# Kernel optimization log

Hardware: AMD Instinct MI355X
Metric: run time of the kernel (lower is better)

Reference implementation:

```python
import jax, jax.numpy as jnp
import numpy as np

BS, NS, S = 4, 16384, 8
C_PLANE, RES = 64, 128
IN_DIM = 3 * C_PLANE  # 192


def _bilerp(plane, uv):
    """plane: [B,C,H,W]; uv: [B,n,2] in [0,1] -> [B,n,C] bilinear samples (border clamp)."""
    B, C, H, W = plane.shape
    x = jnp.clip(uv[..., 0], 0.0, 1.0) * (W - 1)
    y = jnp.clip(uv[..., 1], 0.0, 1.0) * (H - 1)
    x0 = jnp.floor(x).astype(jnp.int32)
    y0 = jnp.floor(y).astype(jnp.int32)
    x1 = jnp.minimum(x0 + 1, W - 1)
    y1 = jnp.minimum(y0 + 1, H - 1)
    wx = (x - x0)[:, :, None]
    wy = (y - y0)[:, :, None]
    gat = jax.vmap(lambda p, yy, xx: p[:, yy, xx].T)  # per-batch gather -> [n,C]
    f00 = gat(plane, y0, x0)
    f01 = gat(plane, y0, x1)
    f10 = gat(plane, y1, x0)
    f11 = gat(plane, y1, x1)
    return (f00 * (1 - wx) * (1 - wy) + f01 * wx * (1 - wy)
            + f10 * (1 - wx) * wy + f11 * wx * wy)


def _sample_triplane(p, feat_xz, feat_xy, feat_yz):
    """p: [B,n,3] -> concat of bilinear samples from the three planes: [B,n,3C]."""
    f_xz = _bilerp(feat_xz, p[..., jnp.array([0, 2])])
    f_xy = _bilerp(feat_xy, p[..., jnp.array([0, 1])])
    f_yz = _bilerp(feat_yz, p[..., jnp.array([1, 2])])
    return jnp.concatenate([f_xz, f_xy, f_yz], axis=-1)


def setup_inputs() -> dict:
    key = jax.random.key(0)
    ks = jax.random.split(key, 12)
    w = 0.05  # small init so predicted offsets stay near the query point
    return {
        "query_pos": jax.random.uniform(ks[0], (BS, NS, 3), dtype=jnp.float32),
        "feat_xz": jax.random.normal(ks[1], (BS, C_PLANE, RES, RES), dtype=jnp.float32),
        "feat_xy": jax.random.normal(ks[2], (BS, C_PLANE, RES, RES), dtype=jnp.float32),
        "feat_yz": jax.random.normal(ks[3], (BS, C_PLANE, RES, RES), dtype=jnp.float32),
        "W_v": jax.random.normal(ks[4], (IN_DIM, IN_DIM), dtype=jnp.float32) * w,
        "b_v": jnp.zeros((IN_DIM,), jnp.float32),
        "W_out": jax.random.normal(ks[5], (IN_DIM, IN_DIM), dtype=jnp.float32) * w,
        "b_out": jnp.zeros((IN_DIM,), jnp.float32),
        "W_off": jax.random.normal(ks[6], (3 * S, IN_DIM), dtype=jnp.float32) * w,
        "b_off": jnp.zeros((3 * S,), jnp.float32),
        "W_wt": jax.random.normal(ks[7], (S, IN_DIM), dtype=jnp.float32) * w,
        "b_wt": jnp.zeros((S,), jnp.float32),
    }


def reference(query_pos, feat_xz, feat_xy, feat_yz, W_v, b_v, W_out, b_out,
              W_off, b_off, W_wt, b_wt):
    bs, ns, _ = query_pos.shape
    # feature at query points: [bs, ns, IN_DIM]
    feature = _sample_triplane(query_pos, feat_xz, feat_xy, feat_yz)
    # predicted per-sample offsets and weights
    off = (feature @ W_off.T + b_off).reshape(bs, ns, S, 3)
    wt = (feature @ W_wt.T + b_wt)[..., None]            # [bs, ns, S, 1]
    pts = off + query_pos[:, :, None, :]                  # [bs, ns, S, 3]
    # gather features at offset locations: [bs, ns*S, IN_DIM]
    aux = _sample_triplane(pts.reshape(bs, ns * S, 3), feat_xz, feat_xy, feat_yz)
    v = (aux @ W_v.T + b_v).reshape(bs, ns, S, -1)        # [bs, ns, S, hidden]
    out = (v * wt).sum(axis=-2)                           # weighted sum over samples
    out = out @ W_out.T + b_out + feature                 # residual add
    return out  # [bs, ns, IN_DIM]
```

## Files before the change

### kernel.cpp

```cpp
#include <hip/hip_runtime.h>

#define BS 4
#define NS 16384
#define S_SAMP 8
#define CPL 64
#define RES 128
#define IN_DIM 192
#define NPTS (BS * NS)
#define PL_STRIDE (RES * RES * CPL)
#define PLANES_T_FLOATS (BS * 3 * PL_STRIDE)

__global__ __launch_bounds__(256) void transpose_planes(
    const float* __restrict__ xz, const float* __restrict__ xy,
    const float* __restrict__ yz, float* __restrict__ T) {
  __shared__ float tile[64][33];
  int blk = blockIdx.x;
  int xt = blk & 3;
  int y  = (blk >> 2) & 127;
  int pl = (blk >> 9) % 3;
  int b  = blk / 1536;
  const float* src = (pl == 0) ? xz : ((pl == 1) ? xy : yz);
  src += (size_t)b * CPL * RES * RES + (size_t)y * RES + xt * 32;
  int tid = threadIdx.x;
  int xl = tid & 31, c0 = tid >> 5;
#pragma unroll
  for (int r = 0; r < 8; ++r) {
    int c = c0 + (r << 3);
    tile[c][xl] = src[(size_t)c * RES * RES + xl];
  }
  __syncthreads();
  float* dst = T + ((size_t)(b * 3 + pl) * RES * RES + (size_t)y * RES + xt * 32) * CPL;
  int c2 = tid & 63, x0 = tid >> 6;
#pragma unroll
  for (int r = 0; r < 8; ++r) {
    int xl2 = x0 + (r << 2);
    dst[(size_t)xl2 * CPL + c2] = tile[c2][xl2];
  }
}

__global__ __launch_bounds__(192) void precompute_wc(
    const float* __restrict__ W_v, const float* __restrict__ b_v,
    const float* __restrict__ W_out, float* __restrict__ WcT,
    float* __restrict__ bc) {
  int j = threadIdx.x;
  int k = blockIdx.x;
  if (k < IN_DIM) {
    float acc = 0.f;
    for (int m = 0; m < IN_DIM; ++m)
      acc += W_out[j * IN_DIM + m] * W_v[m * IN_DIM + k];
    WcT[k * IN_DIM + j] = acc;
  } else {
    float acc = 0.f;
    for (int m = 0; m < IN_DIM; ++m)
      acc += W_out[j * IN_DIM + m] * b_v[m];
    bc[j] = acc;
  }
}

__device__ __forceinline__ float bilerp_s(const float* __restrict__ pb, float u,
                                          float v, int lane) {
  u = fminf(fmaxf(u, 0.f), 1.f) * 127.f;
  v = fminf(fmaxf(v, 0.f), 1.f) * 127.f;
  float xf = floorf(u), yf = floorf(v);
  float wx = u - xf, wy = v - yf;
  int x0 = __builtin_amdgcn_readfirstlane((int)xf);
  int y0 = __builtin_amdgcn_readfirstlane((int)yf);
  int dx = (x0 < 127) ? CPL : 0;
  int dy = (y0 < 127) ? RES * CPL : 0;
  const float* b00 = pb + (((y0 << 7) + x0) << 6);
  float f00 = b00[lane];
  float f01 = b00[dx + lane];
  float f10 = b00[dy + lane];
  float f11 = b00[dy + dx + lane];
  float fx0 = f00 + wx * (f01 - f00);
  float fx1 = f10 + wx * (f11 - f10);
  return fx0 + wy * (fx1 - fx0);
}

__global__ __launch_bounds__(256, 4) void fused_sample(
    const float* __restrict__ qpos, const float* __restrict__ planesT,
    const float* __restrict__ W_off, const float* __restrict__ b_off,
    const float* __restrict__ W_wt, const float* __restrict__ b_wt,
    float* __restrict__ waux, float* __restrict__ swtg,
    float* __restrict__ featg) {
  __shared__ float feat_lds[4][IN_DIM];
  __shared__ float offwt[4][32];
  int w = threadIdx.x >> 6, lane = threadIdx.x & 63;
  int p = (blockIdx.x << 2) + w;
  int b = p >> 14;
  float qx = qpos[p * 3 + 0], qy = qpos[p * 3 + 1], qz = qpos[p * 3 + 2];
  const float* Tb = planesT + (size_t)b * 3 * PL_STRIDE;

  float f0 = bilerp_s(Tb, qx, qz, lane);
  float f1 = bilerp_s(Tb + PL_STRIDE, qx, qy, lane);
  float f2 = bilerp_s(Tb + 2 * PL_STRIDE, qy, qz, lane);
  feat_lds[w][lane] = f0;
  feat_lds[w][64 + lane] = f1;
  feat_lds[w][128 + lane] = f2;
  __syncthreads();

  {
    int oj = lane & 31;
    const float* row = (oj < 24) ? (W_off + oj * IN_DIM)
                                 : (W_wt + (oj - 24) * IN_DIM);
    float bias = (oj < 24) ? b_off[oj] : b_wt[oj - 24];
    int k0 = (lane >> 5) * 96;
    const float4* r4 = (const float4*)(row + k0);
    float a0 = 0.f, a1 = 0.f, a2 = 0.f, a3 = 0.f;
#pragma unroll
    for (int k4 = 0; k4 < 24; ++k4) {
      float4 rv = r4[k4];
      a0 += rv.x * feat_lds[w][k0 + 4 * k4 + 0];
      a1 += rv.y * feat_lds[w][k0 + 4 * k4 + 1];
      a2 += rv.z * feat_lds[w][k0 + 4 * k4 + 2];
      a3 += rv.w * feat_lds[w][k0 + 4 * k4 + 3];
    }
    float acc = (a0 + a1) + (a2 + a3);
    acc += __shfl_xor(acc, 32);
    if (lane < 32) offwt[w][oj] = acc + bias;
  }
  __syncthreads();

  float wa0 = 0.f, wa1 = 0.f, wa2 = 0.f, swt = 0.f;
#pragma unroll 4
  for (int s = 0; s < S_SAMP; ++s) {
    float wt = offwt[w][24 + s];
    float px = qx + offwt[w][3 * s + 0];
    float py = qy + offwt[w][3 * s + 1];
    float pz = qz + offwt[w][3 * s + 2];
    wa0 += wt * bilerp_s(Tb, px, pz, lane);
    wa1 += wt * bilerp_s(Tb + PL_STRIDE, px, py, lane);
    wa2 += wt * bilerp_s(Tb + 2 * PL_STRIDE, py, pz, lane);
    swt += wt;
  }

  size_t o = (size_t)p * IN_DIM + lane;
  waux[o] = wa0; waux[o + 64] = wa1; waux[o + 128] = wa2;
  if (lane == 0) swtg[p] = swt;
  featg[o] = f0; featg[o + 64] = f1; featg[o + 128] = f2;
}

__global__ __launch_bounds__(512) void out_gemm(
    const float* __restrict__ waux, const float* __restrict__ swtg,
    const float* __restrict__ WcT, const float* __restrict__ bc,
    const float* __restrict__ b_out, float* __restrict__ out) {
  __shared__ float wtile[64 * IN_DIM];
  int tid = threadIdx.x;
  int w = tid >> 6, lane = tid & 63;
  int p0 = blockIdx.x * 128 + w * 16;

  float acc[4][4][3] = {};
  for (int c = 0; c < 3; ++c) {
#pragma unroll
    for (int r = 0; r < 24; ++r)
      wtile[tid + r * 512] = WcT[c * 64 * IN_DIM + tid + r * 512];
    __syncthreads();
#pragma unroll
    for (int g = 0; g < 4; ++g) {
      const float* wrow[4];
#pragma unroll
      for (int q = 0; q < 4; ++q)
        wrow[q] = waux +
                  (size_t)__builtin_amdgcn_readfirstlane(p0 + g * 4 + q) * IN_DIM +
                  c * 64;
#pragma unroll 4
      for (int k = 0; k < 64; ++k) {
        float v0 = wtile[k * IN_DIM + lane];
        float v1 = wtile[k * IN_DIM + 64 + lane];
        float v2 = wtile[k * IN_DIM + 128 + lane];
#pragma unroll
        for (int q = 0; q < 4; ++q) {
          float wv = wrow[q][k];
          acc[g][q][0] += v0 * wv;
          acc[g][q][1] += v1 * wv;
          acc[g][q][2] += v2 * wv;
        }
      }
    }
    __syncthreads();
  }
#pragma unroll
  for (int g = 0; g < 4; ++g)
#pragma unroll
    for (int q = 0; q < 4; ++q) {
      int p = p0 + g * 4 + q;
      float sw = swtg[p];
#pragma unroll
      for (int t = 0; t < 3; ++t) {
        int j = lane + t * 64;
        size_t o = (size_t)p * IN_DIM + j;
        out[o] = acc[g][q][t] + sw * bc[j] + b_out[j] + out[o];
      }
    }
}

extern "C" void kernel_launch(void* const* d_in, const int* in_sizes, int n_in,
                              void* d_out, int out_size, void* d_ws,
                              size_t ws_size, hipStream_t stream) {
  const float* qpos  = (const float*)d_in[0];
  const float* xz    = (const float*)d_in[1];
  const float* xy    = (const float*)d_in[2];
  const float* yz    = (const float*)d_in[3];
  const float* W_v   = (const float*)d_in[4];
  const float* b_v   = (const float*)d_in[5];
  const float* W_out = (const float*)d_in[6];
  const float* b_out = (const float*)d_in[7];
  const float* W_off = (const float*)d_in[8];
  const float* b_off = (const float*)d_in[9];
  const float* W_wt  = (const float*)d_in[10];
  const float* b_wt  = (const float*)d_in[11];

  float* ws      = (float*)d_ws;
  float* planesT = ws;
  float* waux    = planesT + PLANES_T_FLOATS;
  float* swtg    = waux + (size_t)NPTS * IN_DIM;
  float* WcT     = swtg + NPTS;
  float* bc      = WcT + IN_DIM * IN_DIM;
  float* out     = (float*)d_out;

  hipLaunchKernelGGL(transpose_planes, dim3(BS * 3 * RES * 4), dim3(256), 0,
                     stream, xz, xy, yz, planesT);
  hipLaunchKernelGGL(precompute_wc, dim3(IN_DIM + 1), dim3(IN_DIM), 0, stream,
                     W_v, b_v, W_out, WcT, bc);
  hipLaunchKernelGGL(fused_sample, dim3(NPTS / 4), dim3(256), 0, stream, qpos,
                     planesT, W_off, b_off, W_wt, b_wt, waux, swtg, out);
  hipLaunchKernelGGL(out_gemm, dim3(NPTS / 128), dim3(512), 0, stream, waux,
                     swtg, WcT, bc, b_out, out);
}
```

Measured before the change: 484.6 us.

## Process two points per wave in sampler and restage output GEMM tiles

The sampling kernel now handles two query points per wavefront and issues all 24 bilinear corner loads before interpolating, to expose more memory-level parallelism. The offset/weight projection gives each half-wave a full 192-length dot product, which removes the cross-lane shuffle. The output GEMM now stages a 64-point activation tile in LDS and streams WcT rows from global memory, replacing the earlier staging of weight tiles. precompute_wc swaps its block and thread indices so that W_v reads coalesce. The extra in-flight loads raise register pressure and may lower occupancy.

```diff
diff --git a/kernel.cpp b/kernel.cpp
--- a/kernel.cpp
+++ b/kernel.cpp
@@ -42,9 +42,9 @@
     const float* __restrict__ W_v, const float* __restrict__ b_v,
     const float* __restrict__ W_out, float* __restrict__ WcT,
     float* __restrict__ bc) {
-  int j = threadIdx.x;
-  int k = blockIdx.x;
-  if (k < IN_DIM) {
+  int j = blockIdx.x;
+  int k = threadIdx.x;
+  if (j < IN_DIM) {
     float acc = 0.f;
     for (int m = 0; m < IN_DIM; ++m)
       acc += W_out[j * IN_DIM + m] * W_v[m * IN_DIM + k];
@@ -52,29 +52,24 @@
   } else {
     float acc = 0.f;
     for (int m = 0; m < IN_DIM; ++m)
-      acc += W_out[j * IN_DIM + m] * b_v[m];
-    bc[j] = acc;
-  }
-}
-
-__device__ __forceinline__ float bilerp_s(const float* __restrict__ pb, float u,
-                                          float v, int lane) {
+      acc += W_out[k * IN_DIM + m] * b_v[m];
+    bc[k] = acc;
+  }
+}
+
+__device__ __forceinline__ void mkaddr(const float* __restrict__ pb, float u,
+                                       float v, const float*& b00, int& dx,
+                                       int& dy, float& wx, float& wy) {
   u = fminf(fmaxf(u, 0.f), 1.f) * 127.f;
   v = fminf(fmaxf(v, 0.f), 1.f) * 127.f;
   float xf = floorf(u), yf = floorf(v);
-  float wx = u - xf, wy = v - yf;
+  wx = u - xf;
+  wy = v - yf;
   int x0 = __builtin_amdgcn_readfirstlane((int)xf);
   int y0 = __builtin_amdgcn_readfirstlane((int)yf);
-  int dx = (x0 < 127) ? CPL : 0;
-  int dy = (y0 < 127) ? RES * CPL : 0;
-  const float* b00 = pb + (((y0 << 7) + x0) << 6);
-  float f00 = b00[lane];
-  float f01 = b00[dx + lane];
-  float f10 = b00[dy + lane];
-  float f11 = b00[dy + dx + lane];
-  float fx0 = f00 + wx * (f01 - f00);
-  float fx1 = f10 + wx * (f11 - f10);
-  return fx0 + wy * (fx1 - fx0);
+  dx = (x0 < 127) ? CPL : 0;
+  dy = (y0 < 127) ? RES * CPL : 0;
+  b00 = pb + (((y0 << 7) + x0) << 6);
 }
 
 __global__ __launch_bounds__(256, 4) void fused_sample(
@@ -83,115 +78,176 @@
     const float* __restrict__ W_wt, const float* __restrict__ b_wt,
     float* __restrict__ waux, float* __restrict__ swtg,
     float* __restrict__ featg) {
-  __shared__ float feat_lds[4][IN_DIM];
-  __shared__ float offwt[4][32];
+  __shared__ float feat_lds[8][IN_DIM];
+  __shared__ float offwt[8][32];
   int w = threadIdx.x >> 6, lane = threadIdx.x & 63;
-  int p = (blockIdx.x << 2) + w;
-  int b = p >> 14;
-  float qx = qpos[p * 3 + 0], qy = qpos[p * 3 + 1], qz = qpos[p * 3 + 2];
-  const float* Tb = planesT + (size_t)b * 3 * PL_STRIDE;
-
-  float f0 = bilerp_s(Tb, qx, qz, lane);
-  float f1 = bilerp_s(Tb + PL_STRIDE, qx, qy, lane);
-  float f2 = bilerp_s(Tb + 2 * PL_STRIDE, qy, qz, lane);
-  feat_lds[w][lane] = f0;
-  feat_lds[w][64 + lane] = f1;
-  feat_lds[w][128 + lane] = f2;
-  __syncthreads();
-
+  int p0 = blockIdx.x * 8 + w * 2;
+  int p1 = p0 + 1;
+  int b0 = p0 >> 14, b1 = p1 >> 14;
+  float qx0 = qpos[p0 * 3 + 0], qy0 = qpos[p0 * 3 + 1], qz0 = qpos[p0 * 3 + 2];
+  float qx1 = qpos[p1 * 3 + 0], qy1 = qpos[p1 * 3 + 1], qz1 = qpos[p1 * 3 + 2];
+  const float* Tb0 = planesT + (size_t)b0 * 3 * PL_STRIDE;
+  const float* Tb1 = planesT + (size_t)b1 * 3 * PL_STRIDE;
+
+  float f[6];
   {
-    int oj = lane & 31;
+    const float* B[6]; int DX[6], DY[6]; float WX[6], WY[6];
+    mkaddr(Tb0,                 qx0, qz0, B[0], DX[0], DY[0], WX[0], WY[0]);
+    mkaddr(Tb0 + PL_STRIDE,     qx0, qy0, B[1], DX[1], DY[1], WX[1], WY[1]);
+    mkaddr(Tb0 + 2 * PL_STRIDE, qy0, qz0, B[2], DX[2], DY[2], WX[2], WY[2]);
+    mkaddr(Tb1,                 qx1, qz1, B[3], DX[3], DY[3], WX[3], WY[3]);
+    mkaddr(Tb1 + PL_STRIDE,     qx1, qy1, B[4], DX[4], DY[4], WX[4], WY[4]);
+    mkaddr(Tb1 + 2 * PL_STRIDE, qy1, qz1, B[5], DX[5], DY[5], WX[5], WY[5]);
+    float t00[6], t01[6], t10[6], t11[6];
+#pragma unroll
+    for (int i = 0; i < 6; ++i) {
+      t00[i] = B[i][lane];
+      t01[i] = B[i][DX[i] + lane];
+      t10[i] = B[i][DY[i] + lane];
+      t11[i] = B[i][DY[i] + DX[i] + lane];
+    }
+#pragma unroll
+    for (int i = 0; i < 6; ++i) {
+      float a = t00[i] + WX[i] * (t01[i] - t00[i]);
+      float c = t10[i] + WX[i] * (t11[i] - t10[i]);
+      f[i] = a + WY[i] * (c - a);
+    }
+  }
+  feat_lds[w * 2 + 0][lane] = f[0];
+  feat_lds[w * 2 + 0][64 + lane] = f[1];
+  feat_lds[w * 2 + 0][128 + lane] = f[2];
+  feat_lds[w * 2 + 1][lane] = f[3];
+  feat_lds[w * 2 + 1][64 + lane] = f[4];
+  feat_lds[w * 2 + 1][128 + lane] = f[5];
+  __syncthreads();
+
+  {
+    int pt = lane >> 5, oj = lane & 31;
     const float* row = (oj < 24) ? (W_off + oj * IN_DIM)
                                  : (W_wt + (oj - 24) * IN_DIM);
     float bias = (oj < 24) ? b_off[oj] : b_wt[oj - 24];
-    int k0 = (lane >> 5) * 96;
-    const float4* r4 = (const float4*)(row + k0);
+    const float4* r4 = (const float4*)row;
+    const float4* fl = (const float4*)feat_lds[w * 2 + pt];
     float a0 = 0.f, a1 = 0.f, a2 = 0.f, a3 = 0.f;
 #pragma unroll
-    for (int k4 = 0; k4 < 24; ++k4) {
+    for (int k4 = 0; k4 < IN_DIM / 4; ++k4) {
       float4 rv = r4[k4];
-      a0 += rv.x * feat_lds[w][k0 + 4 * k4 + 0];
-      a1 += rv.y * feat_lds[w][k0 + 4 * k4 + 1];
-      a2 += rv.z * feat_lds[w][k0 + 4 * k4 + 2];
-      a3 += rv.w * feat_lds[w][k0 + 4 * k4 + 3];
-    }
-    float acc = (a0 + a1) + (a2 + a3);
-    acc += __shfl_xor(acc, 32);
-    if (lane < 32) offwt[w][oj] = acc + bias;
-  }
-  __syncthreads();
-
-  float wa0 = 0.f, wa1 = 0.f, wa2 = 0.f, swt = 0.f;
-#pragma unroll 4
+      float4 fv = fl[k4];
+      a0 += rv.x * fv.x;
+      a1 += rv.y * fv.y;
+      a2 += rv.z * fv.z;
+      a3 += rv.w * fv.w;
+    }
+    offwt[w * 2 + pt][oj] = bias + ((a0 + a1) + (a2 + a3));
+  }
+  __syncthreads();
+
+  float wa[2][3] = {};
+  float swt0 = 0.f, swt1 = 0.f;
+#pragma unroll 2
   for (int s = 0; s < S_SAMP; ++s) {
-    float wt = offwt[w][24 + s];
-    float px = qx + offwt[w][3 * s + 0];
-    float py = qy + offwt[w][3 * s + 1];
-    float pz = qz + offwt[w][3 * s + 2];
-    wa0 += wt * bilerp_s(Tb, px, pz, lane);
-    wa1 += wt * bilerp_s(Tb + PL_STRIDE, px, py, lane);
-    wa2 += wt * bilerp_s(Tb + 2 * PL_STRIDE, py, pz, lane);
-    swt += wt;
-  }
-
-  size_t o = (size_t)p * IN_DIM + lane;
-  waux[o] = wa0; waux[o + 64] = wa1; waux[o + 128] = wa2;
-  if (lane == 0) swtg[p] = swt;
-  featg[o] = f0; featg[o + 64] = f1; featg[o + 128] = f2;
-}
-
-__global__ __launch_bounds__(512) void out_gemm(
+    float ox0 = offwt[w * 2 + 0][3 * s + 0];
+    float oy0 = offwt[w * 2 + 0][3 * s + 1];
+    float oz0 = offwt[w * 2 + 0][3 * s + 2];
+    float wt0 = offwt[w * 2 + 0][24 + s];
+    float ox1 = offwt[w * 2 + 1][3 * s + 0];
+    float oy1 = offwt[w * 2 + 1][3 * s + 1];
+    float oz1 = offwt[w * 2 + 1][3 * s + 2];
+    float wt1 = offwt[w * 2 + 1][24 + s];
+    float px0 = qx0 + ox0, py0 = qy0 + oy0, pz0 = qz0 + oz0;
+    float px1 = qx1 + ox1, py1 = qy1 + oy1, pz1 = qz1 + oz1;
+
+    const float* B[6]; int DX[6], DY[6]; float WX[6], WY[6];
+    mkaddr(Tb0,                 px0, pz0, B[0], DX[0], DY[0], WX[0], WY[0]);
+    mkaddr(Tb0 + PL_STRIDE,     px0, py0, B[1], DX[1], DY[1], WX[1], WY[1]);
+    mkaddr(Tb0 + 2 * PL_STRIDE, py0, pz0, B[2], DX[2], DY[2], WX[2], WY[2]);
+    mkaddr(Tb1,                 px1, pz1, B[3], DX[3], DY[3], WX[3], WY[3]);
+    mkaddr(Tb1 + PL_STRIDE,     px1, py1, B[4], DX[4], DY[4], WX[4], WY[4]);
+    mkaddr(Tb1 + 2 * PL_STRIDE, py1, pz1, B[5], DX[5], DY[5], WX[5], WY[5]);
+    float t00[6], t01[6], t10[6], t11[6];
+#pragma unroll
+    for (int i = 0; i < 6; ++i) {
+      t00[i] = B[i][lane];
+      t01[i] = B[i][DX[i] + lane];
+      t10[i] = B[i][DY[i] + lane];
+      t11[i] = B[i][DY[i] + DX[i] + lane];
+    }
+    float r[6];
+#pragma unroll
+    for (int i = 0; i < 6; ++i) {
+      float a = t00[i] + WX[i] * (t01[i] - t00[i]);
+      float c = t10[i] + WX[i] * (t11[i] - t10[i]);
+      r[i] = a + WY[i] * (c - a);
+    }
+    wa[0][0] += wt0 * r[0]; wa[0][1] += wt0 * r[1]; wa[0][2] += wt0 * r[2];
+    wa[1][0] += wt1 * r[3]; wa[1][1] += wt1 * r[4]; wa[1][2] += wt1 * r[5];
+    swt0 += wt0; swt1 += wt1;
+  }
+
+  size_t o0 = (size_t)p0 * IN_DIM + lane;
+  size_t o1 = (size_t)p1 * IN_DIM + lane;
+  waux[o0] = wa[0][0]; waux[o0 + 64] = wa[0][1]; waux[o0 + 128] = wa[0][2];
+  waux[o1] = wa[1][0]; waux[o1 + 64] = wa[1][1]; waux[o1 + 128] = wa[1][2];
+  if (lane == 0) { swtg[p0] = swt0; swtg[p1] = swt1; }
+  featg[o0] = f[0]; featg[o0 + 64] = f[1]; featg[o0 + 128] = f[2];
+  featg[o1] = f[3]; featg[o1 + 64] = f[4]; featg[o1 + 128] = f[5];
+}
+
+__global__ __launch_bounds__(256) void out_gemm(
     const float* __restrict__ waux, const float* __restrict__ swtg,
     const float* __restrict__ WcT, const float* __restrict__ bc,
     const float* __restrict__ b_out, float* __restrict__ out) {
-  __shared__ float wtile[64 * IN_DIM];
+  __shared__ float at[64 * IN_DIM];
   int tid = threadIdx.x;
   int w = tid >> 6, lane = tid & 63;
-  int p0 = blockIdx.x * 128 + w * 16;
-
-  float acc[4][4][3] = {};
+  int p0 = blockIdx.x * 64;
+
+  const float4* src = (const float4*)(waux + (size_t)p0 * IN_DIM);
+  float4* dst4 = (float4*)at;
+#pragma unroll
+  for (int i = 0; i < 12; ++i) dst4[tid + i * 256] = src[tid + i * 256];
+  __syncthreads();
+
+  int pw = w * 16;
+  float acc[16][3] = {};
   for (int c = 0; c < 3; ++c) {
-#pragma unroll
-    for (int r = 0; r < 24; ++r)
-      wtile[tid + r * 512] = WcT[c * 64 * IN_DIM + tid + r * 512];
-    __syncthreads();
-#pragma unroll
-    for (int g = 0; g < 4; ++g) {
-      const float* wrow[4];
-#pragma unroll
-      for (int q = 0; q < 4; ++q)
-        wrow[q] = waux +
-                  (size_t)__builtin_amdgcn_readfirstlane(p0 + g * 4 + q) * IN_DIM +
-                  c * 64;
-#pragma unroll 4
-      for (int k = 0; k < 64; ++k) {
-        float v0 = wtile[k * IN_DIM + lane];
-        float v1 = wtile[k * IN_DIM + 64 + lane];
-        float v2 = wtile[k * IN_DIM + 128 + lane];
-#pragma unroll
-        for (int q = 0; q < 4; ++q) {
-          float wv = wrow[q][k];
-          acc[g][q][0] += v0 * wv;
-          acc[g][q][1] += v1 * wv;
-          acc[g][q][2] += v2 * wv;
-        }
+    const float* wc = WcT + c * 64 * IN_DIM;
+#pragma unroll 2
+    for (int k4 = 0; k4 < 16; ++k4) {
+      float v0[4], v1[4], v2[4];
+#pragma unroll
+      for (int kk = 0; kk < 4; ++kk) {
+        const float* r = wc + (k4 * 4 + kk) * IN_DIM;
+        v0[kk] = r[lane];
+        v1[kk] = r[64 + lane];
+        v2[kk] = r[128 + lane];
       }
-    }
-    __syncthreads();
-  }
-#pragma unroll
-  for (int g = 0; g < 4; ++g)
-#pragma unroll
-    for (int q = 0; q < 4; ++q) {
-      int p = p0 + g * 4 + q;
-      float sw = swtg[p];
-#pragma unroll
-      for (int t = 0; t < 3; ++t) {
-        int j = lane + t * 64;
-        size_t o = (size_t)p * IN_DIM + j;
-        out[o] = acc[g][q][t] + sw * bc[j] + b_out[j] + out[o];
+#pragma unroll
+      for (int q = 0; q < 16; ++q) {
+        float4 a4 = *(const float4*)&at[(pw + q) * IN_DIM + c * 64 + k4 * 4];
+        acc[q][0] += v0[0] * a4.x + v0[1] * a4.y + v0[2] * a4.z + v0[3] * a4.w;
+        acc[q][1] += v1[0] * a4.x + v1[1] * a4.y + v1[2] * a4.z + v1[3] * a4.w;
+        acc[q][2] += v2[0] * a4.x + v2[1] * a4.y + v2[2] * a4.z + v2[3] * a4.w;
       }
     }
+  }
+
+  float bcv[3], bov[3];
+#pragma unroll
+  for (int t = 0; t < 3; ++t) {
+    bcv[t] = bc[lane + t * 64];
+    bov[t] = b_out[lane + t * 64];
+  }
+#pragma unroll
+  for (int q = 0; q < 16; ++q) {
+    int p = p0 + pw + q;
+    float sw = swtg[p];
+#pragma unroll
+    for (int t = 0; t < 3; ++t) {
+      size_t o = (size_t)p * IN_DIM + lane + t * 64;
+      out[o] = acc[q][t] + sw * bcv[t] + bov[t] + out[o];
+    }
+  }
 }
 
 extern "C" void kernel_launch(void* const* d_in, const int* in_sizes, int n_in,
@@ -222,8 +278,8 @@
                      stream, xz, xy, yz, planesT);
   hipLaunchKernelGGL(precompute_wc, dim3(IN_DIM + 1), dim3(IN_DIM), 0, stream,
                      W_v, b_v, W_out, WcT, bc);
-  hipLaunchKernelGGL(fused_sample, dim3(NPTS / 4), dim3(256), 0, stream, qpos,
+  hipLaunchKernelGGL(fused_sample, dim3(NPTS / 8), dim3(256), 0, stream, qpos,
                      planesT, W_off, b_off, W_wt, b_wt, waux, swtg, out);
-  hipLaunchKernelGGL(out_gemm, dim3(NPTS / 128), dim3(512), 0, stream, waux,
+  hipLaunchKernelGGL(out_gemm, dim3(NPTS / 64), dim3(256), 0, stream, waux,
                      swtg, WcT, bc, b_out, out);
 }
```

Measured after the change: 482.2 us. About the same (-0.5%).
